# Kernel tuning notes

Hardware: AMD Instinct MI355X
Metric: run time of the kernel (lower is better)

The kernel has to match this reference:

```python
import jax, jax.numpy as jnp
import numpy as np

B, T, IN, H, C = 256, 128, 64, 512, 11


def setup_inputs() -> dict:
    key = jax.random.key(0)
    ks = jax.random.split(key, 10)
    sc = 1.0 / np.sqrt(H).astype(np.float32)
    def w(k, shape, s):
        return jax.random.normal(k, shape, dtype=jnp.float32) * s
    return {
        "x": jax.random.normal(ks[0], (B, T, IN), dtype=jnp.float32),
        "t": jax.random.uniform(ks[1], (B, T), dtype=jnp.float32),
        # nn.LSTMCell params (gate order i, f, g, o)
        "W_ih": w(ks[2], (4 * H, IN), sc),
        "W_hh": w(ks[3], (4 * H, H), sc),
        "b_ih": jnp.zeros((4 * H,), jnp.float32),
        "b_hh": jnp.zeros((4 * H,), jnp.float32),
        # f_node: Linear(H,H) -> Tanh -> Linear(H,H)
        "W1": w(ks[4], (H, H), sc),
        "b1": jnp.zeros((H,), jnp.float32),
        "W2": w(ks[5], (H, H), sc),
        "b2": jnp.zeros((H,), jnp.float32),
        # ODELSTM per-step output Linear(H, out_feature=H)
        "Wo": w(ks[6], (H, H), sc),
        "bo": jnp.zeros((H,), jnp.float32),
        # model head Linear(H, num_classes)
        "Wc": w(ks[7], (C, H), sc),
        "bc": jnp.zeros((C,), jnp.float32),
    }


def reference(x, t, W_ih, W_hh, b_ih, b_hh, W1, b1, W2, b2, Wo, bo, Wc, bc):
    def f_node(y):  # [B,H] -> [B,H]
        return jnp.tanh(y @ W1.T + b1) @ W2.T + b2

    def rk4(y, dt):  # dt: [B,1]
        k1 = f_node(y)
        k2 = f_node(y + k1 * dt * 0.5)
        k3 = f_node(y + k2 * dt * 0.5)
        k4 = f_node(y + k3 * dt)
        return y + dt * (k1 + 2.0 * k2 + 2.0 * k3 + k4) / 6.0

    def step(carry, inp):
        h, c = carry
        xt, ts = inp  # [B,IN], [B]
        z = xt @ W_ih.T + h @ W_hh.T + (b_ih + b_hh)
        i, f, g, o = jnp.split(z, 4, axis=-1)
        c = jax.nn.sigmoid(f) * c + jax.nn.sigmoid(i) * jnp.tanh(g)
        h = jax.nn.sigmoid(o) * jnp.tanh(c)
        dt = (ts * (1.0 / 3.0))[:, None]  # 3 fixed unfolds per timestep
        for _ in range(3):
            h = rk4(h, dt)
        out = h @ Wo.T + bo  # ODELSTM per-step output projection
        return (h, c), out

    h0 = jnp.zeros((x.shape[0], W_hh.shape[1]), x.dtype)
    (_h, _c), outs = jax.lax.scan(
        step, (h0, h0), (jnp.swapaxes(x, 0, 1), jnp.swapaxes(t, 0, 1))
    )
    outs = jnp.swapaxes(outs, 0, 1)  # [B,T,H]
    return outs @ Wc.T + bc  # [B,T,num_classes]
```

## Files before the change

kernel.cpp:

```cpp
#include <hip/hip_runtime.h>
#include <stdint.h>


#define H_  512
#define B_  256
#define T_  128
#define IN_ 64
#define NC_ 11
#define LD_ 520

typedef _Float16 h8v __attribute__((ext_vector_type(8)));
typedef float    f4v __attribute__((ext_vector_type(4)));
typedef unsigned long long ull;

__device__ __forceinline__ float fsigm(float x) { return 1.0f / (1.0f + __expf(-x)); }
__device__ __forceinline__ float ftanh(float x) { return 1.0f - 2.0f / (1.0f + __expf(2.0f * x)); }


__global__ void prep_M(const float* __restrict__ W1, const float* __restrict__ W2,
                       float* __restrict__ Mtmp) {
  __shared__ float w1s[8][512];
  int tid = threadIdx.x;
  int n0 = blockIdx.x * 8;
  for (int i = tid; i < 8 * 512; i += 256) {
    int nn = i >> 9, m = i & 511;
    w1s[nn][m] = W1[(n0 + nn) * 512 + m];
  }
  __syncthreads();
  float acc0[8] = {0,0,0,0,0,0,0,0}, acc1[8] = {0,0,0,0,0,0,0,0};
  for (int m = 0; m < 512; ++m) {
    float a = W2[m * 512 + tid];
    float b = W2[m * 512 + 256 + tid];
#pragma unroll
    for (int j = 0; j < 8; ++j) { acc0[j] += a * w1s[j][m]; acc1[j] += b * w1s[j][m]; }
  }
  for (int j = 0; j < 8; ++j) {
    Mtmp[(size_t)tid * 512 + n0 + j]         = acc0[j];
    Mtmp[(size_t)(tid + 256) * 512 + n0 + j] = acc1[j];
  }
}

__global__ void prep_small(const float* __restrict__ W1, const float* __restrict__ b2,
                           const float* __restrict__ Wc, const float* __restrict__ Wo,
                           const float* __restrict__ bo, const float* __restrict__ bc,
                           float* __restrict__ dvec, float* __restrict__ Wco,
                           float* __restrict__ bprime) {
  __shared__ float wcs[NC_ * 512];
  int tid = threadIdx.x;
  if (blockIdx.x == 0) {
    for (int n = tid; n < 512; n += 256) {
      float acc = 0.f;
      for (int m = 0; m < 512; ++m) acc += b2[m] * W1[n * 512 + m];
      dvec[n] = acc;
    }
  } else if (blockIdx.x == 1) {
    if (tid < NC_) {
      float acc = bc[tid];
      for (int m = 0; m < 512; ++m) acc += Wc[tid * 512 + m] * bo[m];
      bprime[tid] = acc;
    }
  } else {
    for (int i = tid; i < NC_ * 512; i += 256) wcs[i] = Wc[i];
    __syncthreads();
    int h = (blockIdx.x - 2) * 256 + tid;
    float acc[NC_];
#pragma unroll
    for (int c = 0; c < NC_; ++c) acc[c] = 0.f;
    for (int m = 0; m < 512; ++m) {
      float wo = Wo[m * 512 + h];
#pragma unroll
      for (int c = 0; c < NC_; ++c) acc[c] += wo * wcs[c * 512 + m];
    }
    for (int c = 0; c < NC_; ++c) Wco[c * 512 + h] = acc[c];
  }
}

__global__ void prep_wtilde(const float* __restrict__ Whh, const float* __restrict__ Wih,
                            _Float16* __restrict__ Wtil) {
  int gidx = blockIdx.x * 256 + threadIdx.x;
  int lane = gidx & 63, fb = gidx >> 6;
  int kc = fb % 18; int t2 = fb / 18;
  int t = t2 & 31, g = t2 >> 5;
  int n = g * 512 + t * 16 + (lane & 15);
  int k = kc * 32 + ((lane >> 4) & 3) * 8;
  _Float16 vals[8];
  if (k < 512) {
#pragma unroll
    for (int j = 0; j < 8; ++j) vals[j] = (_Float16)Whh[(size_t)n * 512 + k + j];
  } else {
#pragma unroll
    for (int j = 0; j < 8; ++j) vals[j] = (_Float16)Wih[(size_t)n * 64 + (k - 512) + j];
  }
  *(h8v*)(Wtil + (size_t)fb * 512 + lane * 8) = *(h8v*)vals;
}

__global__ void prep_fragW(const float* __restrict__ W, _Float16* __restrict__ dst) {
  int gidx = blockIdx.x * 256 + threadIdx.x;
  int lane = gidx & 63, fb = gidx >> 6;
  int t = fb >> 4, kc = fb & 15;
  int n = t * 16 + (lane & 15);
  int k = kc * 32 + ((lane >> 4) & 3) * 8;
  _Float16 vals[8];
#pragma unroll
  for (int j = 0; j < 8; ++j) vals[j] = (_Float16)W[(size_t)n * 512 + k + j];
  *(h8v*)(dst + (size_t)fb * 512 + lane * 8) = *(h8v*)vals;
}

__global__ void prep_fragM(const float* __restrict__ Mtmp, _Float16* __restrict__ dst) {
  int gidx = blockIdx.x * 256 + threadIdx.x;
  int lane = gidx & 63, fb = gidx >> 6;
  int t = fb >> 4, kc = fb & 15;
  int n = t * 16 + (lane & 15);
  int k = kc * 32 + ((lane >> 4) & 3) * 8;
  _Float16 vals[8];
#pragma unroll
  for (int j = 0; j < 8; ++j) vals[j] = (_Float16)Mtmp[(size_t)(k + j) * 512 + n];
  *(h8v*)(dst + (size_t)fb * 512 + lane * 8) = *(h8v*)vals;
}


__device__ __forceinline__ void phase_exchange(int* __restrict__ cnt,
                                               ull* __restrict__ Xb,
                                               _Float16* __restrict__ ACT,
                                               int s, int target) {
  const int tid = threadIdx.x;
  __syncthreads();
  {
    int m = tid >> 4, ch = tid & 15;
    ull v = *(const ull*)(ACT + m * LD_ + s * 64 + ch * 4);
    __hip_atomic_store(Xb + m * 128 + s * 16 + ch, v,
                       __ATOMIC_RELAXED, __HIP_MEMORY_SCOPE_AGENT);
  }
  __builtin_amdgcn_s_waitcnt(0);
  __syncthreads();
  if (tid == 0)
    __hip_atomic_fetch_add(cnt, 1, __ATOMIC_RELAXED, __HIP_MEMORY_SCOPE_AGENT);
  int v;
  do {
    v = __hip_atomic_load(cnt, __ATOMIC_RELAXED, __HIP_MEMORY_SCOPE_AGENT);
    if (v < target) __builtin_amdgcn_s_sleep(2);
  } while (v < target);
  __asm__ volatile("" ::: "memory");
  ull tv[8];
#pragma unroll
  for (int i = 0; i < 8; ++i) {
    int idx = i * 256 + tid;
    int os = idx >> 8, r = idx & 255, m = r >> 4, ch = r & 15;
    tv[i] = __hip_atomic_load(Xb + m * 128 + os * 16 + ch,
                              __ATOMIC_RELAXED, __HIP_MEMORY_SCOPE_AGENT);
  }
#pragma unroll
  for (int i = 0; i < 8; ++i) {
    int idx = i * 256 + tid;
    int os = idx >> 8, r = idx & 255, m = r >> 4, ch = r & 15;
    *(ull*)(ACT + m * LD_ + os * 64 + ch * 4) = tv[i];
  }
  __syncthreads();
}

__device__ __forceinline__ f4v mm_lds(const _Float16* __restrict__ ACT,
                                      const _Float16* __restrict__ Ws,
                                      int w, int lane) {
  f4v e = {0,0,0,0}, o = {0,0,0,0};
  const _Float16* arow = ACT + (lane & 15) * LD_ + (lane >> 4) * 8;
  const h8v* b = (const h8v*)Ws;
#pragma unroll
  for (int kc = 0; kc < 16; kc += 2) {
    e = __builtin_amdgcn_mfma_f32_16x16x32_f16(*(const h8v*)(arow + kc * 32),
                                               b[(w * 16 + kc) * 64 + lane], e, 0, 0, 0);
    o = __builtin_amdgcn_mfma_f32_16x16x32_f16(*(const h8v*)(arow + (kc + 1) * 32),
                                               b[(w * 16 + kc + 1) * 64 + lane], o, 0, 0, 0);
  }
  return e + o;
}

__device__ __forceinline__ f4v mm_reg(const _Float16* __restrict__ ACT,
                                      const h8v* __restrict__ mreg, int lane) {
  f4v e = {0,0,0,0}, o = {0,0,0,0};
  const _Float16* arow = ACT + (lane & 15) * LD_ + (lane >> 4) * 8;
#pragma unroll
  for (int kc = 0; kc < 16; kc += 2) {
    e = __builtin_amdgcn_mfma_f32_16x16x32_f16(*(const h8v*)(arow + kc * 32),
                                               mreg[kc], e, 0, 0, 0);
    o = __builtin_amdgcn_mfma_f32_16x16x32_f16(*(const h8v*)(arow + (kc + 1) * 32),
                                               mreg[kc + 1], o, 0, 0, 0);
  }
  return e + o;
}

__launch_bounds__(256, 1)
__global__ void recur(const float* __restrict__ x,
                      const float* __restrict__ tin,
                      const float* __restrict__ bih,
                      const float* __restrict__ bhh,
                      const float* __restrict__ b1g,
                      const float* __restrict__ b2g,
                      const _Float16* __restrict__ Wtil,
                      const _Float16* __restrict__ W1T,
                      const _Float16* __restrict__ W2T,
                      const _Float16* __restrict__ MF,
                      const float* __restrict__ dvec,
                      _Float16* __restrict__ Hsave,
                      ull* __restrict__ Xchg,
                      int* __restrict__ flags) {
  const int blk = blockIdx.x, c = blk & 15, s = blk >> 4;
  const int tid = threadIdx.x, w = tid >> 6, lane = tid & 63;
  const int lm = lane & 15, quad = lane >> 4;
  const int col = s * 64 + w * 16 + lm;

  __shared__ __align__(16) _Float16 W1s[4 * 16 * 512];
  __shared__ __align__(16) _Float16 W2s[4 * 16 * 512];
  __shared__ __align__(16) _Float16 ACT[16 * LD_];

  {
    const h8v* g1 = (const h8v*)(W1T + (size_t)s * 32768);
    const h8v* g2 = (const h8v*)(W2T + (size_t)s * 32768);
    h8v* l1 = (h8v*)W1s; h8v* l2 = (h8v*)W2s;
    for (int i = tid; i < 4096; i += 256) { l1[i] = g1[i]; l2[i] = g2[i]; }
  }
  h8v mreg[16];
  {
    const h8v* gm = (const h8v*)(MF + ((size_t)(4 * s + w) * 16) * 512);
#pragma unroll
    for (int kc = 0; kc < 16; ++kc) mreg[kc] = gm[kc * 64 + lane];
  }
  for (int i = tid; i < 16 * LD_; i += 256) ACT[i] = (_Float16)0.f;

  const float zb0 = bih[col] + bhh[col];
  const float zb1 = bih[512 + col] + bhh[512 + col];
  const float zb2 = bih[1024 + col] + bhh[1024 + col];
  const float zb3 = bih[1536 + col] + bhh[1536 + col];
  const float b1r = b1g[col], dvr = dvec[col], b2r = b2g[col];

  float c_[4] = {0,0,0,0}, h_[4] = {0,0,0,0};
  float u1a[4], SSa[4], SMa[4];
  int phase = 0;
  int* cnt = flags + c * 32;
  __syncthreads();

  for (int ts = 0; ts < T_; ++ts) {
    float dt_[4];
#pragma unroll
    for (int r = 0; r < 4; ++r)
      dt_[r] = tin[(c * 16 + quad * 4 + r) * T_ + ts] * (1.0f / 3.0f);

    {
      f4v z0 = {0,0,0,0}, z1 = {0,0,0,0}, z2 = {0,0,0,0}, z3 = {0,0,0,0};
      const _Float16* arow = ACT + lm * LD_ + quad * 8;
      const h8v* wt = (const h8v*)Wtil;
      const int tb = 4 * s + w;
#pragma unroll
      for (int kc = 0; kc < 16; ++kc) {
        h8v av = *(const h8v*)(arow + kc * 32);
        z0 = __builtin_amdgcn_mfma_f32_16x16x32_f16(av, wt[(size_t)((0 * 32 + tb) * 18 + kc) * 64 + lane], z0, 0, 0, 0);
        z1 = __builtin_amdgcn_mfma_f32_16x16x32_f16(av, wt[(size_t)((1 * 32 + tb) * 18 + kc) * 64 + lane], z1, 0, 0, 0);
        z2 = __builtin_amdgcn_mfma_f32_16x16x32_f16(av, wt[(size_t)((2 * 32 + tb) * 18 + kc) * 64 + lane], z2, 0, 0, 0);
        z3 = __builtin_amdgcn_mfma_f32_16x16x32_f16(av, wt[(size_t)((3 * 32 + tb) * 18 + kc) * 64 + lane], z3, 0, 0, 0);
      }
      const float* xr = x + ((size_t)(c * 16 + lm) * T_ + ts) * IN_ + quad * 8;
#pragma unroll
      for (int kx = 0; kx < 2; ++kx) {
        float4 f0 = *(const float4*)(xr + kx * 32);
        float4 f1 = *(const float4*)(xr + kx * 32 + 4);
        h8v av;
        av[0] = (_Float16)f0.x; av[1] = (_Float16)f0.y; av[2] = (_Float16)f0.z; av[3] = (_Float16)f0.w;
        av[4] = (_Float16)f1.x; av[5] = (_Float16)f1.y; av[6] = (_Float16)f1.z; av[7] = (_Float16)f1.w;
        int kc = 16 + kx;
        z0 = __builtin_amdgcn_mfma_f32_16x16x32_f16(av, wt[(size_t)((0 * 32 + tb) * 18 + kc) * 64 + lane], z0, 0, 0, 0);
        z1 = __builtin_amdgcn_mfma_f32_16x16x32_f16(av, wt[(size_t)((1 * 32 + tb) * 18 + kc) * 64 + lane], z1, 0, 0, 0);
        z2 = __builtin_amdgcn_mfma_f32_16x16x32_f16(av, wt[(size_t)((2 * 32 + tb) * 18 + kc) * 64 + lane], z2, 0, 0, 0);
        z3 = __builtin_amdgcn_mfma_f32_16x16x32_f16(av, wt[(size_t)((3 * 32 + tb) * 18 + kc) * 64 + lane], z3, 0, 0, 0);
      }
      __syncthreads();
#pragma unroll
      for (int r = 0; r < 4; ++r) {
        float zi = z0[r] + zb0, zf = z1[r] + zb1, zg = z2[r] + zb2, zo = z3[r] + zb3;
        float cv = fsigm(zf) * c_[r] + fsigm(zi) * ftanh(zg);
        c_[r] = cv;
        h_[r] = fsigm(zo) * ftanh(cv);
        ACT[(quad * 4 + r) * LD_ + col] = (_Float16)h_[r];
      }
    }
    ++phase;
    phase_exchange(cnt, Xchg + (size_t)((phase & 1) * 16 + c) * 2048, ACT, s, 8 * phase);

    {
      f4v D = mm_lds(ACT, W1s, w, lane);
      __syncthreads();
#pragma unroll
      for (int r = 0; r < 4; ++r) {
        float uv = D[r] + b1r;
        u1a[r] = uv;
        float t1v = ftanh(uv);
        SSa[r] = t1v;
        ACT[(quad * 4 + r) * LD_ + col] = (_Float16)t1v;
      }
    }
    ++phase;
    phase_exchange(cnt, Xchg + (size_t)((phase & 1) * 16 + c) * 2048, ACT, s, 8 * phase);

#pragma unroll 1
    for (int uf = 0; uf < 3; ++uf) {
      {
        f4v D = mm_reg(ACT, mreg, lane);
        __syncthreads();
#pragma unroll
        for (int r = 0; r < 4; ++r) {
          float Dv = D[r];
          float u2 = u1a[r] + 0.5f * dt_[r] * (Dv + dvr);
          SMa[r] = Dv;
          float t2v = ftanh(u2);
          SSa[r] += 2.0f * t2v;
          ACT[(quad * 4 + r) * LD_ + col] = (_Float16)t2v;
        }
      }
      ++phase;
      phase_exchange(cnt, Xchg + (size_t)((phase & 1) * 16 + c) * 2048, ACT, s, 8 * phase);

      {
        f4v D = mm_reg(ACT, mreg, lane);
        __syncthreads();
#pragma unroll
        for (int r = 0; r < 4; ++r) {
          float Dv = D[r];
          float u3 = u1a[r] + 0.5f * dt_[r] * (Dv + dvr);
          SMa[r] += 2.0f * Dv;
          float t3v = ftanh(u3);
          SSa[r] += 2.0f * t3v;
          ACT[(quad * 4 + r) * LD_ + col] = (_Float16)t3v;
        }
      }
      ++phase;
      phase_exchange(cnt, Xchg + (size_t)((phase & 1) * 16 + c) * 2048, ACT, s, 8 * phase);

      {
        f4v D = mm_reg(ACT, mreg, lane);
        __syncthreads();
#pragma unroll
        for (int r = 0; r < 4; ++r) {
          float Dv = D[r];
          float u4 = u1a[r] + dt_[r] * (Dv + dvr);
          SMa[r] += 2.0f * Dv;
          float t4v = ftanh(u4);
          SSa[r] += t4v;
          ACT[(quad * 4 + r) * LD_ + col] = (uf < 2) ? (_Float16)t4v : (_Float16)SSa[r];
        }
      }
      ++phase;
      phase_exchange(cnt, Xchg + (size_t)((phase & 1) * 16 + c) * 2048, ACT, s, 8 * phase);

      if (uf < 2) {
        f4v D = mm_reg(ACT, mreg, lane);
        __syncthreads();
#pragma unroll
        for (int r = 0; r < 4; ++r) {
          float Dv = D[r];
          SMa[r] += Dv;
          float un = u1a[r] + (dt_[r] * (1.0f / 6.0f)) * SMa[r] + dt_[r] * dvr;
          u1a[r] = un;
          float t1v = ftanh(un);
          SSa[r] += t1v;
          ACT[(quad * 4 + r) * LD_ + col] = (_Float16)t1v;
        }
        ++phase;
        phase_exchange(cnt, Xchg + (size_t)((phase & 1) * 16 + c) * 2048, ACT, s, 8 * phase);
      }
    }

    {
      f4v D = mm_lds(ACT, W2s, w, lane);
      __syncthreads();
#pragma unroll
      for (int r = 0; r < 4; ++r) {
        h_[r] += (dt_[r] * (1.0f / 6.0f)) * D[r] + (3.0f * dt_[r]) * b2r;
        _Float16 hv = (_Float16)h_[r];
        ACT[(quad * 4 + r) * LD_ + col] = hv;
        Hsave[((size_t)(ts + 1) * B_ + c * 16 + quad * 4 + r) * H_ + col] = hv;
      }
    }
    ++phase;
    phase_exchange(cnt, Xchg + (size_t)((phase & 1) * 16 + c) * 2048, ACT, s, 8 * phase);
  }
}

__global__ void final_out(const _Float16* __restrict__ Hsave,
                          const float* __restrict__ Wco,
                          const float* __restrict__ bprime,
                          float* __restrict__ out) {
  __shared__ float wcs[NC_][520];
  int tid = threadIdx.x;
  for (int i = tid; i < NC_ * 512; i += 256) wcs[i >> 9][i & 511] = Wco[i];
  __syncthreads();
  int r0 = blockIdx.x * 64;
  int rl = tid >> 4, cc = tid & 15;
  for (int pass = 0; pass < 4; ++pass) {
    int row = r0 + pass * 16 + rl;
    int b = row >> 7, t = row & 127;
    const _Float16* hrow = Hsave + ((size_t)(t + 1) * B_ + b) * H_;
    if (cc < NC_) {
      float acc = 0.f;
      for (int k8 = 0; k8 < 64; ++k8) {
        h8v hv = *(const h8v*)(hrow + k8 * 8);
#pragma unroll
        for (int j = 0; j < 8; ++j) acc += (float)hv[j] * wcs[cc][k8 * 8 + j];
      }
      out[(size_t)row * NC_ + cc] = acc + bprime[cc];
    }
  }
}

extern "C" void kernel_launch(void* const* d_in, const int* in_sizes, int n_in,
                              void* d_out, int out_size, void* d_ws, size_t ws_size,
                              hipStream_t stream) {
  (void)in_sizes; (void)n_in; (void)out_size; (void)ws_size;
  const float* x   = (const float*)d_in[0];
  const float* tin = (const float*)d_in[1];
  const float* Wih = (const float*)d_in[2];
  const float* Whh = (const float*)d_in[3];
  const float* bih = (const float*)d_in[4];
  const float* bhh = (const float*)d_in[5];
  const float* W1  = (const float*)d_in[6];
  const float* b1  = (const float*)d_in[7];
  const float* W2  = (const float*)d_in[8];
  const float* b2  = (const float*)d_in[9];
  const float* Wo  = (const float*)d_in[10];
  const float* bo  = (const float*)d_in[11];
  const float* Wc  = (const float*)d_in[12];
  const float* bc  = (const float*)d_in[13];

  char* ws = (char*)d_ws;
  size_t off = 0;
  auto alloc = [&](size_t bytes) -> void* {
    void* p = ws + off;
    off = (off + bytes + 1023) & ~(size_t)1023;
    return p;
  };
  _Float16* Wtil  = (_Float16*)alloc((size_t)2304 * 512 * 2);
  _Float16* W1T   = (_Float16*)alloc((size_t)512 * 512 * 2);
  _Float16* W2T   = (_Float16*)alloc((size_t)512 * 512 * 2);
  _Float16* MF    = (_Float16*)alloc((size_t)512 * 512 * 2);
  float*    Mtmp  = (float*)alloc((size_t)512 * 512 * 4);
  float*    dvec  = (float*)alloc(512 * 4);
  float*    WcoF  = (float*)alloc((size_t)NC_ * 512 * 4);
  float*    bprim = (float*)alloc(64);
  _Float16* Hsave = (_Float16*)alloc((size_t)(T_ + 1) * B_ * H_ * 2);
  ull*      Xchg  = (ull*)alloc((size_t)2 * 16 * 2048 * 8);
  int*      flags = (int*)alloc(16 * 32 * 4);

  hipMemsetAsync(flags, 0, 16 * 32 * 4, stream);

  prep_M<<<64, 256, 0, stream>>>(W1, W2, Mtmp);
  prep_small<<<4, 256, 0, stream>>>(W1, b2, Wc, Wo, bo, bc, dvec, WcoF, bprim);
  prep_wtilde<<<576, 256, 0, stream>>>(Whh, Wih, Wtil);
  prep_fragW<<<128, 256, 0, stream>>>(W1, W1T);
  prep_fragW<<<128, 256, 0, stream>>>(W2, W2T);
  prep_fragM<<<128, 256, 0, stream>>>(Mtmp, MF);
  recur<<<128, 256, 0, stream>>>(x, tin, bih, bhh, b1, b2, Wtil, W1T, W2T, MF,
                                 dvec, Hsave, Xchg, flags);
  final_out<<<512, 256, 0, stream>>>(Hsave, WcoF, bprim, (float*)d_out);
}
```

Measured before the change: 5.057 ms.

## Use XCC-local plain exchange, single-thread spin wait, and MFMA-fragment activation layout

At startup each block records its XCC id, and the blocks check whether every group of 8 blocks sharing a batch chunk sits on the same XCC. When they do, the inter-block exchange uses volatile plain loads and stores in place of agent-scope atomics. The spin wait on the counter is now done by thread 0 alone, followed by a barrier. Activations are stored in LDS directly in MFMA A-fragment order, so the matmul operand loads become simple lane-indexed vector reads. The risks are coherence correctness of non-atomic loads across CUs and extra 32-bit scatter stores when writing the fragment layout.

```diff
diff --git a/kernel.cpp b/kernel.cpp
--- a/kernel.cpp
+++ b/kernel.cpp
@@ -7,7 +7,6 @@
 #define T_  128
 #define IN_ 64
 #define NC_ 11
-#define LD_ 520
 
 typedef _Float16 h8v __attribute__((ext_vector_type(8)));
 typedef float    f4v __attribute__((ext_vector_type(4)));
@@ -119,71 +118,85 @@
 }
 
 
-__device__ __forceinline__ void phase_exchange(int* __restrict__ cnt,
+__device__ __forceinline__ int af_idx(int m, int col) {
+  return (col >> 5) * 512 + ((m & 15) + ((col >> 3) & 3) * 16) * 8 + (col & 7);
+}
+
+__device__ __forceinline__ void phase_exchange(bool fast, int* __restrict__ cnt,
                                                ull* __restrict__ Xb,
-                                               _Float16* __restrict__ ACT,
+                                               _Float16* __restrict__ AF,
                                                int s, int target) {
   const int tid = threadIdx.x;
   __syncthreads();
   {
     int m = tid >> 4, ch = tid & 15;
-    ull v = *(const ull*)(ACT + m * LD_ + s * 64 + ch * 4);
-    __hip_atomic_store(Xb + m * 128 + s * 16 + ch, v,
-                       __ATOMIC_RELAXED, __HIP_MEMORY_SCOPE_AGENT);
+    int c0 = s * 64 + ch * 4;
+    const uint32_t* src = (const uint32_t*)(AF + af_idx(m, c0));
+    ull v = ((ull)src[1] << 32) | (ull)src[0];
+    ull* dst = Xb + m * 128 + s * 16 + ch;
+    if (fast) *(volatile ull*)dst = v;
+    else __hip_atomic_store(dst, v, __ATOMIC_RELAXED, __HIP_MEMORY_SCOPE_AGENT);
   }
   __builtin_amdgcn_s_waitcnt(0);
   __syncthreads();
-  if (tid == 0)
+  if (tid == 0) {
     __hip_atomic_fetch_add(cnt, 1, __ATOMIC_RELAXED, __HIP_MEMORY_SCOPE_AGENT);
-  int v;
-  do {
-    v = __hip_atomic_load(cnt, __ATOMIC_RELAXED, __HIP_MEMORY_SCOPE_AGENT);
-    if (v < target) __builtin_amdgcn_s_sleep(2);
-  } while (v < target);
-  __asm__ volatile("" ::: "memory");
+    int v;
+    do {
+      v = __hip_atomic_load(cnt, __ATOMIC_RELAXED, __HIP_MEMORY_SCOPE_AGENT);
+      if (v < target) __builtin_amdgcn_s_sleep(1);
+    } while (v < target);
+  }
+  __syncthreads();
   ull tv[8];
+  if (fast) {
+#pragma unroll
+    for (int i = 0; i < 8; ++i) {
+      int idx = i * 256 + tid, os = idx >> 8, r = idx & 255, m = r >> 4, ch = r & 15;
+      tv[i] = *(volatile const ull*)(Xb + m * 128 + os * 16 + ch);
+    }
+  } else {
+#pragma unroll
+    for (int i = 0; i < 8; ++i) {
+      int idx = i * 256 + tid, os = idx >> 8, r = idx & 255, m = r >> 4, ch = r & 15;
+      tv[i] = __hip_atomic_load(Xb + m * 128 + os * 16 + ch,
+                                __ATOMIC_RELAXED, __HIP_MEMORY_SCOPE_AGENT);
+    }
+  }
 #pragma unroll
   for (int i = 0; i < 8; ++i) {
-    int idx = i * 256 + tid;
-    int os = idx >> 8, r = idx & 255, m = r >> 4, ch = r & 15;
-    tv[i] = __hip_atomic_load(Xb + m * 128 + os * 16 + ch,
-                              __ATOMIC_RELAXED, __HIP_MEMORY_SCOPE_AGENT);
-  }
-#pragma unroll
-  for (int i = 0; i < 8; ++i) {
-    int idx = i * 256 + tid;
-    int os = idx >> 8, r = idx & 255, m = r >> 4, ch = r & 15;
-    *(ull*)(ACT + m * LD_ + os * 64 + ch * 4) = tv[i];
-  }
-  __syncthreads();
-}
-
-__device__ __forceinline__ f4v mm_lds(const _Float16* __restrict__ ACT,
+    int idx = i * 256 + tid, os = idx >> 8, r = idx & 255, m = r >> 4, ch = r & 15;
+    int c0 = os * 64 + ch * 4;
+    uint32_t* d = (uint32_t*)(AF + af_idx(m, c0));
+    d[0] = (uint32_t)tv[i]; d[1] = (uint32_t)(tv[i] >> 32);
+  }
+  __syncthreads();
+}
+
+__device__ __forceinline__ f4v mm_lds(const _Float16* __restrict__ AF,
                                       const _Float16* __restrict__ Ws,
                                       int w, int lane) {
   f4v e = {0,0,0,0}, o = {0,0,0,0};
-  const _Float16* arow = ACT + (lane & 15) * LD_ + (lane >> 4) * 8;
+  const h8v* a = (const h8v*)AF;
   const h8v* b = (const h8v*)Ws;
 #pragma unroll
   for (int kc = 0; kc < 16; kc += 2) {
-    e = __builtin_amdgcn_mfma_f32_16x16x32_f16(*(const h8v*)(arow + kc * 32),
+    e = __builtin_amdgcn_mfma_f32_16x16x32_f16(a[kc * 64 + lane],
                                                b[(w * 16 + kc) * 64 + lane], e, 0, 0, 0);
-    o = __builtin_amdgcn_mfma_f32_16x16x32_f16(*(const h8v*)(arow + (kc + 1) * 32),
+    o = __builtin_amdgcn_mfma_f32_16x16x32_f16(a[(kc + 1) * 64 + lane],
                                                b[(w * 16 + kc + 1) * 64 + lane], o, 0, 0, 0);
   }
   return e + o;
 }
 
-__device__ __forceinline__ f4v mm_reg(const _Float16* __restrict__ ACT,
+__device__ __forceinline__ f4v mm_reg(const _Float16* __restrict__ AF,
                                       const h8v* __restrict__ mreg, int lane) {
   f4v e = {0,0,0,0}, o = {0,0,0,0};
-  const _Float16* arow = ACT + (lane & 15) * LD_ + (lane >> 4) * 8;
+  const h8v* a = (const h8v*)AF;
 #pragma unroll
   for (int kc = 0; kc < 16; kc += 2) {
-    e = __builtin_amdgcn_mfma_f32_16x16x32_f16(*(const h8v*)(arow + kc * 32),
-                                               mreg[kc], e, 0, 0, 0);
-    o = __builtin_amdgcn_mfma_f32_16x16x32_f16(*(const h8v*)(arow + (kc + 1) * 32),
-                                               mreg[kc + 1], o, 0, 0, 0);
+    e = __builtin_amdgcn_mfma_f32_16x16x32_f16(a[kc * 64 + lane], mreg[kc], e, 0, 0, 0);
+    o = __builtin_amdgcn_mfma_f32_16x16x32_f16(a[(kc + 1) * 64 + lane], mreg[kc + 1], o, 0, 0, 0);
   }
   return e + o;
 }
@@ -210,7 +223,8 @@
 
   __shared__ __align__(16) _Float16 W1s[4 * 16 * 512];
   __shared__ __align__(16) _Float16 W2s[4 * 16 * 512];
-  __shared__ __align__(16) _Float16 ACT[16 * LD_];
+  __shared__ __align__(16) _Float16 AF[16 * 512];
+  __shared__ int fastsh;
 
   {
     const h8v* g1 = (const h8v*)(W1T + (size_t)s * 32768);
@@ -224,13 +238,38 @@
 #pragma unroll
     for (int kc = 0; kc < 16; ++kc) mreg[kc] = gm[kc * 64 + lane];
   }
-  for (int i = tid; i < 16 * LD_; i += 256) ACT[i] = (_Float16)0.f;
+  for (int i = tid; i < 1024; i += 256) ((uint4*)AF)[i] = make_uint4(0, 0, 0, 0);
+
+  {
+    int xcc = 0;
+    __asm__ volatile("s_getreg_b32 %0, hwreg(HW_REG_XCC_ID)" : "=s"(xcc));
+    int* probes = flags + 512;
+    int* pgcnt  = flags + 512 + 128;
+    int* pmask  = flags + 512 + 129;
+    if (tid == 0) {
+      __hip_atomic_store(&probes[c * 8 + s], xcc, __ATOMIC_RELAXED, __HIP_MEMORY_SCOPE_AGENT);
+      __hip_atomic_fetch_or(pmask, 1 << (xcc & 31), __ATOMIC_RELAXED, __HIP_MEMORY_SCOPE_AGENT);
+      __builtin_amdgcn_s_waitcnt(0);
+      __hip_atomic_fetch_add(pgcnt, 1, __ATOMIC_RELAXED, __HIP_MEMORY_SCOPE_AGENT);
+      while (__hip_atomic_load(pgcnt, __ATOMIC_RELAXED, __HIP_MEMORY_SCOPE_AGENT) < 128)
+        __builtin_amdgcn_s_sleep(4);
+      int e0 = __hip_atomic_load(&probes[c * 8], __ATOMIC_RELAXED, __HIP_MEMORY_SCOPE_AGENT);
+      int eq = 1;
+      for (int i = 1; i < 8; ++i)
+        eq &= (__hip_atomic_load(&probes[c * 8 + i], __ATOMIC_RELAXED, __HIP_MEMORY_SCOPE_AGENT) == e0);
+      int mk = __hip_atomic_load(pmask, __ATOMIC_RELAXED, __HIP_MEMORY_SCOPE_AGENT);
+      fastsh = (eq && __popc((unsigned)mk) >= 2) ? 1 : 0;
+    }
+  }
+  __syncthreads();
+  const bool fast = (fastsh != 0);
 
   const float zb0 = bih[col] + bhh[col];
   const float zb1 = bih[512 + col] + bhh[512 + col];
   const float zb2 = bih[1024 + col] + bhh[1024 + col];
   const float zb3 = bih[1536 + col] + bhh[1536 + col];
   const float b1r = b1g[col], dvr = dvec[col], b2r = b2g[col];
+  const int eb = af_idx(quad * 4, col);
 
   float c_[4] = {0,0,0,0}, h_[4] = {0,0,0,0};
   float u1a[4], SSa[4], SMa[4];
@@ -246,12 +285,12 @@
 
     {
       f4v z0 = {0,0,0,0}, z1 = {0,0,0,0}, z2 = {0,0,0,0}, z3 = {0,0,0,0};
-      const _Float16* arow = ACT + lm * LD_ + quad * 8;
+      const h8v* a = (const h8v*)AF;
       const h8v* wt = (const h8v*)Wtil;
       const int tb = 4 * s + w;
 #pragma unroll
       for (int kc = 0; kc < 16; ++kc) {
-        h8v av = *(const h8v*)(arow + kc * 32);
+        h8v av = a[kc * 64 + lane];
         z0 = __builtin_amdgcn_mfma_f32_16x16x32_f16(av, wt[(size_t)((0 * 32 + tb) * 18 + kc) * 64 + lane], z0, 0, 0, 0);
         z1 = __builtin_amdgcn_mfma_f32_16x16x32_f16(av, wt[(size_t)((1 * 32 + tb) * 18 + kc) * 64 + lane], z1, 0, 0, 0);
         z2 = __builtin_amdgcn_mfma_f32_16x16x32_f16(av, wt[(size_t)((2 * 32 + tb) * 18 + kc) * 64 + lane], z2, 0, 0, 0);
@@ -278,14 +317,14 @@
         float cv = fsigm(zf) * c_[r] + fsigm(zi) * ftanh(zg);
         c_[r] = cv;
         h_[r] = fsigm(zo) * ftanh(cv);
-        ACT[(quad * 4 + r) * LD_ + col] = (_Float16)h_[r];
+        AF[eb + r * 8] = (_Float16)h_[r];
       }
     }
     ++phase;
-    phase_exchange(cnt, Xchg + (size_t)((phase & 1) * 16 + c) * 2048, ACT, s, 8 * phase);
+    phase_exchange(fast, cnt, Xchg + (size_t)((phase & 1) * 16 + c) * 2048, AF, s, 8 * phase);
 
     {
-      f4v D = mm_lds(ACT, W1s, w, lane);
+      f4v D = mm_lds(AF, W1s, w, lane);
       __syncthreads();
 #pragma unroll
       for (int r = 0; r < 4; ++r) {
@@ -293,16 +332,16 @@
         u1a[r] = uv;
         float t1v = ftanh(uv);
         SSa[r] = t1v;
-        ACT[(quad * 4 + r) * LD_ + col] = (_Float16)t1v;
+        AF[eb + r * 8] = (_Float16)t1v;
       }
     }
     ++phase;
-    phase_exchange(cnt, Xchg + (size_t)((phase & 1) * 16 + c) * 2048, ACT, s, 8 * phase);
+    phase_exchange(fast, cnt, Xchg + (size_t)((phase & 1) * 16 + c) * 2048, AF, s, 8 * phase);
 
 #pragma unroll 1
     for (int uf = 0; uf < 3; ++uf) {
       {
-        f4v D = mm_reg(ACT, mreg, lane);
+        f4v D = mm_reg(AF, mreg, lane);
         __syncthreads();
 #pragma unroll
         for (int r = 0; r < 4; ++r) {
@@ -311,14 +350,14 @@
           SMa[r] = Dv;
           float t2v = ftanh(u2);
           SSa[r] += 2.0f * t2v;
-          ACT[(quad * 4 + r) * LD_ + col] = (_Float16)t2v;
+          AF[eb + r * 8] = (_Float16)t2v;
         }
       }
       ++phase;
-      phase_exchange(cnt, Xchg + (size_t)((phase & 1) * 16 + c) * 2048, ACT, s, 8 * phase);
+      phase_exchange(fast, cnt, Xchg + (size_t)((phase & 1) * 16 + c) * 2048, AF, s, 8 * phase);
 
       {
-        f4v D = mm_reg(ACT, mreg, lane);
+        f4v D = mm_reg(AF, mreg, lane);
         __syncthreads();
 #pragma unroll
         for (int r = 0; r < 4; ++r) {
@@ -327,14 +366,14 @@
           SMa[r] += 2.0f * Dv;
           float t3v = ftanh(u3);
           SSa[r] += 2.0f * t3v;
-          ACT[(quad * 4 + r) * LD_ + col] = (_Float16)t3v;
+          AF[eb + r * 8] = (_Float16)t3v;
         }
       }
       ++phase;
-      phase_exchange(cnt, Xchg + (size_t)((phase & 1) * 16 + c) * 2048, ACT, s, 8 * phase);
+      phase_exchange(fast, cnt, Xchg + (size_t)((phase & 1) * 16 + c) * 2048, AF, s, 8 * phase);
 
       {
-        f4v D = mm_reg(ACT, mreg, lane);
+        f4v D = mm_reg(AF, mreg, lane);
         __syncthreads();
 #pragma unroll
         for (int r = 0; r < 4; ++r) {
@@ -343,14 +382,14 @@
           SMa[r] += 2.0f * Dv;
           float t4v = ftanh(u4);
           SSa[r] += t4v;
-          ACT[(quad * 4 + r) * LD_ + col] = (uf < 2) ? (_Float16)t4v : (_Float16)SSa[r];
+          AF[eb + r * 8] = (uf < 2) ? (_Float16)t4v : (_Float16)SSa[r];
         }
       }
       ++phase;
-      phase_exchange(cnt, Xchg + (size_t)((phase & 1) * 16 + c) * 2048, ACT, s, 8 * phase);
+      phase_exchange(fast, cnt, Xchg + (size_t)((phase & 1) * 16 + c) * 2048, AF, s, 8 * phase);
 
       if (uf < 2) {
-        f4v D = mm_reg(ACT, mreg, lane);
+        f4v D = mm_reg(AF, mreg, lane);
         __syncthreads();
 #pragma unroll
         for (int r = 0; r < 4; ++r) {
@@ -360,26 +399,26 @@
           u1a[r] = un;
           float t1v = ftanh(un);
           SSa[r] += t1v;
-          ACT[(quad * 4 + r) * LD_ + col] = (_Float16)t1v;
+          AF[eb + r * 8] = (_Float16)t1v;
         }
         ++phase;
-        phase_exchange(cnt, Xchg + (size_t)((phase & 1) * 16 + c) * 2048, ACT, s, 8 * phase);
+        phase_exchange(fast, cnt, Xchg + (size_t)((phase & 1) * 16 + c) * 2048, AF, s, 8 * phase);
       }
     }
 
     {
-      f4v D = mm_lds(ACT, W2s, w, lane);
+      f4v D = mm_lds(AF, W2s, w, lane);
       __syncthreads();
 #pragma unroll
       for (int r = 0; r < 4; ++r) {
         h_[r] += (dt_[r] * (1.0f / 6.0f)) * D[r] + (3.0f * dt_[r]) * b2r;
         _Float16 hv = (_Float16)h_[r];
-        ACT[(quad * 4 + r) * LD_ + col] = hv;
+        AF[eb + r * 8] = hv;
         Hsave[((size_t)(ts + 1) * B_ + c * 16 + quad * 4 + r) * H_ + col] = hv;
       }
     }
     ++phase;
-    phase_exchange(cnt, Xchg + (size_t)((phase & 1) * 16 + c) * 2048, ACT, s, 8 * phase);
+    phase_exchange(fast, cnt, Xchg + (size_t)((phase & 1) * 16 + c) * 2048, AF, s, 8 * phase);
   }
 }
 
@@ -445,9 +484,9 @@
   float*    bprim = (float*)alloc(64);
   _Float16* Hsave = (_Float16*)alloc((size_t)(T_ + 1) * B_ * H_ * 2);
   ull*      Xchg  = (ull*)alloc((size_t)2 * 16 * 2048 * 8);
-  int*      flags = (int*)alloc(16 * 32 * 4);
-
-  hipMemsetAsync(flags, 0, 16 * 32 * 4, stream);
+  int*      flags = (int*)alloc((512 + 192) * 4);
+
+  hipMemsetAsync(flags, 0, (512 + 192) * 4, stream);
 
   prep_M<<<64, 256, 0, stream>>>(W1, W2, Mtmp);
   prep_small<<<4, 256, 0, stream>>>(W1, b2, Wc, Wo, bo, bc, dvec, WcoF, bprim);
```

After: 8.481 ms. 67.7% more time.

## Interleave two batch chunks per block to hide cross-block exchange latency

Applied to the files above, without the earlier changes.

Each persistent block of the recurrence kernel now handles two 16-row batch chunks and alternates between them. The exchange is split into a publish step and a later gather step, so one chunk's compute runs while its partner chunk's peers finish publishing. W2 moves from LDS into registers, and the grid shrinks from 128 to 64 blocks. The aim is to hide spin-wait and synchronisation latency behind compute, at the cost of half as many blocks, more register pressure, and twice the serial work per block.

```diff
diff --git a/kernel.cpp b/kernel.cpp
--- a/kernel.cpp
+++ b/kernel.cpp
@@ -119,43 +119,45 @@
 }
 
 
-__device__ __forceinline__ void phase_exchange(int* __restrict__ cnt,
-                                               ull* __restrict__ Xb,
-                                               _Float16* __restrict__ ACT,
-                                               int s, int target) {
-  const int tid = threadIdx.x;
-  __syncthreads();
-  {
-    int m = tid >> 4, ch = tid & 15;
-    ull v = *(const ull*)(ACT + m * LD_ + s * 64 + ch * 4);
-    __hip_atomic_store(Xb + m * 128 + s * 16 + ch, v,
-                       __ATOMIC_RELAXED, __HIP_MEMORY_SCOPE_AGENT);
-  }
+__device__ __forceinline__ void gatherX(ull* __restrict__ Xchg, int c,
+                                        int* __restrict__ cnt,
+                                        _Float16* __restrict__ ACT,
+                                        int s, int tid, unsigned ph) {
+  if (ph == 0) return;
+  if (tid == 0) {
+    int target = 8 * (int)ph;
+    while (__hip_atomic_load(cnt, __ATOMIC_RELAXED, __HIP_MEMORY_SCOPE_AGENT) < target)
+      __builtin_amdgcn_s_sleep(1);
+  }
+  __syncthreads();
+  ull* Xb = Xchg + (size_t)((ph & 1) * 16 + c) * 2048;
+  const int m = tid >> 4, ch = tid & 15;
+  ull tv[8];
+#pragma unroll
+  for (int i = 0; i < 8; ++i)
+    tv[i] = __hip_atomic_load(Xb + m * 128 + i * 16 + ch,
+                              __ATOMIC_RELAXED, __HIP_MEMORY_SCOPE_AGENT);
+#pragma unroll
+  for (int i = 0; i < 8; ++i)
+    if (i != s)
+      *(ull*)(ACT + m * LD_ + i * 64 + ch * 4) = tv[i];
+  __syncthreads();
+}
+
+__device__ __forceinline__ void publishX(ull* __restrict__ Xchg, int c,
+                                         int* __restrict__ cnt,
+                                         const _Float16* __restrict__ ACT,
+                                         int s, int tid, unsigned phNew) {
+  __syncthreads();
+  ull* Xb = Xchg + (size_t)((phNew & 1) * 16 + c) * 2048;
+  const int m = tid >> 4, ch = tid & 15;
+  ull v = *(const ull*)(ACT + m * LD_ + s * 64 + ch * 4);
+  __hip_atomic_store(Xb + m * 128 + s * 16 + ch, v,
+                     __ATOMIC_RELAXED, __HIP_MEMORY_SCOPE_AGENT);
   __builtin_amdgcn_s_waitcnt(0);
   __syncthreads();
   if (tid == 0)
     __hip_atomic_fetch_add(cnt, 1, __ATOMIC_RELAXED, __HIP_MEMORY_SCOPE_AGENT);
-  int v;
-  do {
-    v = __hip_atomic_load(cnt, __ATOMIC_RELAXED, __HIP_MEMORY_SCOPE_AGENT);
-    if (v < target) __builtin_amdgcn_s_sleep(2);
-  } while (v < target);
-  __asm__ volatile("" ::: "memory");
-  ull tv[8];
-#pragma unroll
-  for (int i = 0; i < 8; ++i) {
-    int idx = i * 256 + tid;
-    int os = idx >> 8, r = idx & 255, m = r >> 4, ch = r & 15;
-    tv[i] = __hip_atomic_load(Xb + m * 128 + os * 16 + ch,
-                              __ATOMIC_RELAXED, __HIP_MEMORY_SCOPE_AGENT);
-  }
-#pragma unroll
-  for (int i = 0; i < 8; ++i) {
-    int idx = i * 256 + tid;
-    int os = idx >> 8, r = idx & 255, m = r >> 4, ch = r & 15;
-    *(ull*)(ACT + m * LD_ + os * 64 + ch * 4) = tv[i];
-  }
-  __syncthreads();
 }
 
 __device__ __forceinline__ f4v mm_lds(const _Float16* __restrict__ ACT,
@@ -175,15 +177,15 @@
 }
 
 __device__ __forceinline__ f4v mm_reg(const _Float16* __restrict__ ACT,
-                                      const h8v* __restrict__ mreg, int lane) {
+                                      const h8v* __restrict__ reg, int lane) {
   f4v e = {0,0,0,0}, o = {0,0,0,0};
   const _Float16* arow = ACT + (lane & 15) * LD_ + (lane >> 4) * 8;
 #pragma unroll
   for (int kc = 0; kc < 16; kc += 2) {
     e = __builtin_amdgcn_mfma_f32_16x16x32_f16(*(const h8v*)(arow + kc * 32),
-                                               mreg[kc], e, 0, 0, 0);
+                                               reg[kc], e, 0, 0, 0);
     o = __builtin_amdgcn_mfma_f32_16x16x32_f16(*(const h8v*)(arow + (kc + 1) * 32),
-                                               mreg[kc + 1], o, 0, 0, 0);
+                                               reg[kc + 1], o, 0, 0, 0);
   }
   return e + o;
 }
@@ -203,28 +205,29 @@
                       _Float16* __restrict__ Hsave,
                       ull* __restrict__ Xchg,
                       int* __restrict__ flags) {
-  const int blk = blockIdx.x, c = blk & 15, s = blk >> 4;
+  const int blk = blockIdx.x;
+  const int j = blk & 7, s = blk >> 3;
   const int tid = threadIdx.x, w = tid >> 6, lane = tid & 63;
   const int lm = lane & 15, quad = lane >> 4;
   const int col = s * 64 + w * 16 + lm;
+  const int cidx[2] = {2 * j, 2 * j + 1};
 
   __shared__ __align__(16) _Float16 W1s[4 * 16 * 512];
-  __shared__ __align__(16) _Float16 W2s[4 * 16 * 512];
-  __shared__ __align__(16) _Float16 ACT[16 * LD_];
+  __shared__ __align__(16) _Float16 ACTs[2][16 * LD_];
 
   {
     const h8v* g1 = (const h8v*)(W1T + (size_t)s * 32768);
-    const h8v* g2 = (const h8v*)(W2T + (size_t)s * 32768);
-    h8v* l1 = (h8v*)W1s; h8v* l2 = (h8v*)W2s;
-    for (int i = tid; i < 4096; i += 256) { l1[i] = g1[i]; l2[i] = g2[i]; }
-  }
-  h8v mreg[16];
+    h8v* l1 = (h8v*)W1s;
+    for (int i = tid; i < 4096; i += 256) l1[i] = g1[i];
+  }
+  h8v mreg[16], w2reg[16];
   {
-    const h8v* gm = (const h8v*)(MF + ((size_t)(4 * s + w) * 16) * 512);
-#pragma unroll
-    for (int kc = 0; kc < 16; ++kc) mreg[kc] = gm[kc * 64 + lane];
-  }
-  for (int i = tid; i < 16 * LD_; i += 256) ACT[i] = (_Float16)0.f;
+    const h8v* gm = (const h8v*)(MF  + ((size_t)(4 * s + w) * 16) * 512);
+    const h8v* g2 = (const h8v*)(W2T + ((size_t)(4 * s + w) * 16) * 512);
+#pragma unroll
+    for (int kc = 0; kc < 16; ++kc) { mreg[kc] = gm[kc * 64 + lane]; w2reg[kc] = g2[kc * 64 + lane]; }
+  }
+  for (int i = tid; i < 2 * 16 * LD_; i += 256) ACTs[0][i] = (_Float16)0.f;
 
   const float zb0 = bih[col] + bhh[col];
   const float zb1 = bih[512 + col] + bhh[512 + col];
@@ -232,19 +235,23 @@
   const float zb3 = bih[1536 + col] + bhh[1536 + col];
   const float b1r = b1g[col], dvr = dvec[col], b2r = b2g[col];
 
-  float c_[4] = {0,0,0,0}, h_[4] = {0,0,0,0};
-  float u1a[4], SSa[4], SMa[4];
-  int phase = 0;
-  int* cnt = flags + c * 32;
+  float cS[2][4] = {{0,0,0,0},{0,0,0,0}}, hS[2][4] = {{0,0,0,0},{0,0,0,0}};
+  float u1S[2][4], SSS[2][4], SMS[2][4], dtS[2][4];
+  int* cnts[2] = {flags + cidx[0] * 64, flags + cidx[1] * 64};
+  unsigned ph = 0;
   __syncthreads();
 
   for (int ts = 0; ts < T_; ++ts) {
-    float dt_[4];
-#pragma unroll
-    for (int r = 0; r < 4; ++r)
-      dt_[r] = tin[(c * 16 + quad * 4 + r) * T_ + ts] * (1.0f / 3.0f);
-
-    {
+#pragma unroll
+    for (int kk = 0; kk < 2; ++kk)
+#pragma unroll
+      for (int r = 0; r < 4; ++r)
+        dtS[kk][r] = tin[(cidx[kk] * 16 + quad * 4 + r) * T_ + ts] * (1.0f / 3.0f);
+
+#pragma unroll
+    for (int kk = 0; kk < 2; ++kk) {
+      _Float16* ACT = ACTs[kk];
+      gatherX(Xchg, cidx[kk], cnts[kk], ACT, s, tid, ph);
       f4v z0 = {0,0,0,0}, z1 = {0,0,0,0}, z2 = {0,0,0,0}, z3 = {0,0,0,0};
       const _Float16* arow = ACT + lm * LD_ + quad * 8;
       const h8v* wt = (const h8v*)Wtil;
@@ -257,7 +264,7 @@
         z2 = __builtin_amdgcn_mfma_f32_16x16x32_f16(av, wt[(size_t)((2 * 32 + tb) * 18 + kc) * 64 + lane], z2, 0, 0, 0);
         z3 = __builtin_amdgcn_mfma_f32_16x16x32_f16(av, wt[(size_t)((3 * 32 + tb) * 18 + kc) * 64 + lane], z3, 0, 0, 0);
       }
-      const float* xr = x + ((size_t)(c * 16 + lm) * T_ + ts) * IN_ + quad * 8;
+      const float* xr = x + ((size_t)(cidx[kk] * 16 + lm) * T_ + ts) * IN_ + quad * 8;
 #pragma unroll
       for (int kx = 0; kx < 2; ++kx) {
         float4 f0 = *(const float4*)(xr + kx * 32);
@@ -275,111 +282,131 @@
 #pragma unroll
       for (int r = 0; r < 4; ++r) {
         float zi = z0[r] + zb0, zf = z1[r] + zb1, zg = z2[r] + zb2, zo = z3[r] + zb3;
-        float cv = fsigm(zf) * c_[r] + fsigm(zi) * ftanh(zg);
-        c_[r] = cv;
-        h_[r] = fsigm(zo) * ftanh(cv);
-        ACT[(quad * 4 + r) * LD_ + col] = (_Float16)h_[r];
-      }
-    }
-    ++phase;
-    phase_exchange(cnt, Xchg + (size_t)((phase & 1) * 16 + c) * 2048, ACT, s, 8 * phase);
-
-    {
+        float cv = fsigm(zf) * cS[kk][r] + fsigm(zi) * ftanh(zg);
+        cS[kk][r] = cv;
+        hS[kk][r] = fsigm(zo) * ftanh(cv);
+        ACT[(quad * 4 + r) * LD_ + col] = (_Float16)hS[kk][r];
+      }
+      publishX(Xchg, cidx[kk], cnts[kk], ACT, s, tid, ph + 1);
+    }
+    ++ph;
+
+#pragma unroll
+    for (int kk = 0; kk < 2; ++kk) {
+      _Float16* ACT = ACTs[kk];
+      gatherX(Xchg, cidx[kk], cnts[kk], ACT, s, tid, ph);
       f4v D = mm_lds(ACT, W1s, w, lane);
       __syncthreads();
 #pragma unroll
       for (int r = 0; r < 4; ++r) {
         float uv = D[r] + b1r;
-        u1a[r] = uv;
+        u1S[kk][r] = uv;
         float t1v = ftanh(uv);
-        SSa[r] = t1v;
+        SSS[kk][r] = t1v;
         ACT[(quad * 4 + r) * LD_ + col] = (_Float16)t1v;
       }
-    }
-    ++phase;
-    phase_exchange(cnt, Xchg + (size_t)((phase & 1) * 16 + c) * 2048, ACT, s, 8 * phase);
+      publishX(Xchg, cidx[kk], cnts[kk], ACT, s, tid, ph + 1);
+    }
+    ++ph;
 
 #pragma unroll 1
     for (int uf = 0; uf < 3; ++uf) {
-      {
+#pragma unroll
+      for (int kk = 0; kk < 2; ++kk) {
+        _Float16* ACT = ACTs[kk];
+        gatherX(Xchg, cidx[kk], cnts[kk], ACT, s, tid, ph);
         f4v D = mm_reg(ACT, mreg, lane);
         __syncthreads();
 #pragma unroll
         for (int r = 0; r < 4; ++r) {
           float Dv = D[r];
-          float u2 = u1a[r] + 0.5f * dt_[r] * (Dv + dvr);
-          SMa[r] = Dv;
+          float u2 = u1S[kk][r] + 0.5f * dtS[kk][r] * (Dv + dvr);
+          SMS[kk][r] = Dv;
           float t2v = ftanh(u2);
-          SSa[r] += 2.0f * t2v;
+          SSS[kk][r] += 2.0f * t2v;
           ACT[(quad * 4 + r) * LD_ + col] = (_Float16)t2v;
         }
-      }
-      ++phase;
-      phase_exchange(cnt, Xchg + (size_t)((phase & 1) * 16 + c) * 2048, ACT, s, 8 * phase);
-
-      {
+        publishX(Xchg, cidx[kk], cnts[kk], ACT, s, tid, ph + 1);
+      }
+      ++ph;
+
+#pragma unroll
+      for (int kk = 0; kk < 2; ++kk) {
+        _Float16* ACT = ACTs[kk];
+        gatherX(Xchg, cidx[kk], cnts[kk], ACT, s, tid, ph);
         f4v D = mm_reg(ACT, mreg, lane);
         __syncthreads();
 #pragma unroll
         for (int r = 0; r < 4; ++r) {
           float Dv = D[r];
-          float u3 = u1a[r] + 0.5f * dt_[r] * (Dv + dvr);
-          SMa[r] += 2.0f * Dv;
+          float u3 = u1S[kk][r] + 0.5f * dtS[kk][r] * (Dv + dvr);
+          SMS[kk][r] += 2.0f * Dv;
           float t3v = ftanh(u3);
-          SSa[r] += 2.0f * t3v;
+          SSS[kk][r] += 2.0f * t3v;
           ACT[(quad * 4 + r) * LD_ + col] = (_Float16)t3v;
         }
-      }
-      ++phase;
-      phase_exchange(cnt, Xchg + (size_t)((phase & 1) * 16 + c) * 2048, ACT, s, 8 * phase);
-
-      {
+        publishX(Xchg, cidx[kk], cnts[kk], ACT, s, tid, ph + 1);
+      }
+      ++ph;
+
+#pragma unroll
+      for (int kk = 0; kk < 2; ++kk) {
+        _Float16* ACT = ACTs[kk];
+        gatherX(Xchg, cidx[kk], cnts[kk], ACT, s, tid, ph);
         f4v D = mm_reg(ACT, mreg, lane);
         __syncthreads();
 #pragma unroll
         for (int r = 0; r < 4; ++r) {
           float Dv = D[r];
-          float u4 = u1a[r] + dt_[r] * (Dv + dvr);
-          SMa[r] += 2.0f * Dv;
+          float u4 = u1S[kk][r] + dtS[kk][r] * (Dv + dvr);
+          SMS[kk][r] += 2.0f * Dv;
           float t4v = ftanh(u4);
-          SSa[r] += t4v;
-          ACT[(quad * 4 + r) * LD_ + col] = (uf < 2) ? (_Float16)t4v : (_Float16)SSa[r];
+          SSS[kk][r] += t4v;
+          ACT[(quad * 4 + r) * LD_ + col] = (uf < 2) ? (_Float16)t4v : (_Float16)SSS[kk][r];
         }
-      }
-      ++phase;
-      phase_exchange(cnt, Xchg + (size_t)((phase & 1) * 16 + c) * 2048, ACT, s, 8 * phase);
+        publishX(Xchg, cidx[kk], cnts[kk], ACT, s, tid, ph + 1);
+      }
+      ++ph;
 
       if (uf < 2) {
-        f4v D = mm_reg(ACT, mreg, lane);
-        __syncthreads();
-#pragma unroll
-        for (int r = 0; r < 4; ++r) {
-          float Dv = D[r];
-          SMa[r] += Dv;
-          float un = u1a[r] + (dt_[r] * (1.0f / 6.0f)) * SMa[r] + dt_[r] * dvr;
-          u1a[r] = un;
-          float t1v = ftanh(un);
-          SSa[r] += t1v;
-          ACT[(quad * 4 + r) * LD_ + col] = (_Float16)t1v;
+#pragma unroll
+        for (int kk = 0; kk < 2; ++kk) {
+          _Float16* ACT = ACTs[kk];
+          gatherX(Xchg, cidx[kk], cnts[kk], ACT, s, tid, ph);
+          f4v D = mm_reg(ACT, mreg, lane);
+          __syncthreads();
+#pragma unroll
+          for (int r = 0; r < 4; ++r) {
+            float Dv = D[r];
+            SMS[kk][r] += Dv;
+            float un = u1S[kk][r] + (dtS[kk][r] * (1.0f / 6.0f)) * SMS[kk][r] + dtS[kk][r] * dvr;
+            u1S[kk][r] = un;
+            float t1v = ftanh(un);
+            SSS[kk][r] += t1v;
+            ACT[(quad * 4 + r) * LD_ + col] = (_Float16)t1v;
+          }
+          publishX(Xchg, cidx[kk], cnts[kk], ACT, s, tid, ph + 1);
         }
-        ++phase;
-        phase_exchange(cnt, Xchg + (size_t)((phase & 1) * 16 + c) * 2048, ACT, s, 8 * phase);
-      }
-    }
-
-    {
-      f4v D = mm_lds(ACT, W2s, w, lane);
+        ++ph;
+      }
+    }
+
+#pragma unroll
+    for (int kk = 0; kk < 2; ++kk) {
+      _Float16* ACT = ACTs[kk];
+      gatherX(Xchg, cidx[kk], cnts[kk], ACT, s, tid, ph);
+      f4v D = mm_reg(ACT, w2reg, lane);
       __syncthreads();
 #pragma unroll
       for (int r = 0; r < 4; ++r) {
-        h_[r] += (dt_[r] * (1.0f / 6.0f)) * D[r] + (3.0f * dt_[r]) * b2r;
-        _Float16 hv = (_Float16)h_[r];
+        hS[kk][r] += (dtS[kk][r] * (1.0f / 6.0f)) * D[r] + (3.0f * dtS[kk][r]) * b2r;
+        _Float16 hv = (_Float16)hS[kk][r];
         ACT[(quad * 4 + r) * LD_ + col] = hv;
-        Hsave[((size_t)(ts + 1) * B_ + c * 16 + quad * 4 + r) * H_ + col] = hv;
-      }
-    }
-    ++phase;
-    phase_exchange(cnt, Xchg + (size_t)((phase & 1) * 16 + c) * 2048, ACT, s, 8 * phase);
+        Hsave[((size_t)(ts + 1) * B_ + cidx[kk] * 16 + quad * 4 + r) * H_ + col] = hv;
+      }
+      publishX(Xchg, cidx[kk], cnts[kk], ACT, s, tid, ph + 1);
+    }
+    ++ph;
   }
 }
 
@@ -445,9 +472,9 @@
   float*    bprim = (float*)alloc(64);
   _Float16* Hsave = (_Float16*)alloc((size_t)(T_ + 1) * B_ * H_ * 2);
   ull*      Xchg  = (ull*)alloc((size_t)2 * 16 * 2048 * 8);
-  int*      flags = (int*)alloc(16 * 32 * 4);
-
-  hipMemsetAsync(flags, 0, 16 * 32 * 4, stream);
+  int*      flags = (int*)alloc(2048 * 4);
+
+  hipMemsetAsync(flags, 0, 2048 * 4, stream);
 
   prep_M<<<64, 256, 0, stream>>>(W1, W2, Mtmp);
   prep_small<<<4, 256, 0, stream>>>(W1, b2, Wc, Wo, bo, bc, dvec, WcoF, bprim);
@@ -455,7 +482,7 @@
   prep_fragW<<<128, 256, 0, stream>>>(W1, W1T);
   prep_fragW<<<128, 256, 0, stream>>>(W2, W2T);
   prep_fragM<<<128, 256, 0, stream>>>(Mtmp, MF);
-  recur<<<128, 256, 0, stream>>>(x, tin, bih, bhh, b1, b2, Wtil, W1T, W2T, MF,
-                                 dvec, Hsave, Xchg, flags);
+  recur<<<64, 256, 0, stream>>>(x, tin, bih, bhh, b1, b2, Wtil, W1T, W2T, MF,
+                                dvec, Hsave, Xchg, flags);
   final_out<<<512, 256, 0, stream>>>(Hsave, WcoF, bprim, (float*)d_out);
 }
```

Result: slower. 8.405 ms (+66.2%).
